# Optimization experiments

Hardware: AMD Instinct MI355X
Metric: run time of the kernel (lower is better)

## Reference

```python
import jax, jax.numpy as jnp
import numpy as np

N_EMBD = 1024
N_HEAD = 16
BLOCK_SIZE = 2048
NEG_INF = -1e10


def _rope_cache(head_dim, max_positions):
    # theta_i = 10000^{-2i/dim}, freqs[t, i] = t * theta_i
    theta = 1.0 / (10000.0 ** (jnp.arange(0, head_dim, 2, dtype=jnp.float32) / head_dim))
    freqs = jnp.arange(max_positions, dtype=jnp.float32)[:, None] * theta[None, :]
    return jnp.cos(freqs), jnp.sin(freqs)  # each (max_positions, head_dim//2)


def _apply_rope(x, cos, sin):
    # x: (B, nh, T, hs) interpreted as interleaved complex pairs
    B, nh, T, hs = x.shape
    xr = x.reshape(B, nh, T, hs // 2, 2)
    x0, x1 = xr[..., 0], xr[..., 1]
    c = cos[:T][None, None, :, :]
    s = sin[:T][None, None, :, :]
    o0 = x0 * c - x1 * s
    o1 = x0 * s + x1 * c
    return jnp.stack([o0, o1], axis=-1).reshape(B, nh, T, hs)


def setup_inputs() -> dict:
    key = jax.random.key(0)
    ks = jax.random.split(key, 9)
    B, T, C = 2, 2048, N_EMBD
    sc = 1.0 / np.sqrt(C)
    return {
        "x": jax.random.normal(ks[0], (B, T, C), jnp.float32),
        "Wq": jax.random.normal(ks[1], (C, C), jnp.float32) * sc,
        "bq": jax.random.normal(ks[2], (C,), jnp.float32) * 0.02,
        "Wk": jax.random.normal(ks[3], (C, C), jnp.float32) * sc,
        "bk": jax.random.normal(ks[4], (C,), jnp.float32) * 0.02,
        "Wv": jax.random.normal(ks[5], (C, C), jnp.float32) * sc,
        "bv": jax.random.normal(ks[6], (C,), jnp.float32) * 0.02,
        "Wp": jax.random.normal(ks[7], (C, C), jnp.float32) * sc,
        "bp": jax.random.normal(ks[8], (C,), jnp.float32) * 0.02,
    }


def reference(x, Wq, bq, Wk, bk, Wv, bv, Wp, bp):
    B, T, C = x.shape
    nh, hs = N_HEAD, C // N_HEAD

    def heads(W, b):
        return (x @ W.T + b).reshape(B, T, nh, hs).transpose(0, 2, 1, 3)

    q = heads(Wq, bq)
    k = heads(Wk, bk)
    v = heads(Wv, bv)

    cos, sin = _rope_cache(hs, BLOCK_SIZE)
    q = _apply_rope(q, cos, sin)
    k = _apply_rope(k, cos, sin)

    att = jnp.einsum("bhqd,bhkd->bhqk", q, k) * (1.0 / np.sqrt(hs))
    causal = jnp.tril(jnp.ones((T, T), dtype=bool))
    att = jnp.where(causal[None, None], att, NEG_INF)
    att = jax.nn.softmax(att, axis=-1)
    y = jnp.einsum("bhqk,bhkd->bhqd", att, v)
    y = y.transpose(0, 2, 1, 3).reshape(B, T, C)
    return y @ Wp.T + bp
```

## Files before the change

kernel.cpp:

```cpp
#include <hip/hip_runtime.h>

typedef __bf16 bf16;
typedef short  s16;
typedef s16   s16x8 __attribute__((ext_vector_type(8)));
typedef bf16  bf16x4 __attribute__((ext_vector_type(4)));
typedef float f32x4 __attribute__((ext_vector_type(4)));

#define B_SZ 2
#define T_SEQ 2048
#define C_DIM 1024
#define NH 16
#define HS 64
#define M_TOT (B_SZ * T_SEQ)

#define NEG_BIG (-30000.0f)
#define LOG2_10000 13.287712379549449f
#define Q_PRESCALE 0.18033688011112042f

__device__ __forceinline__ float san(float x) {
    unsigned u = __float_as_uint(x);
    return ((u & 0x7F800000u) == 0x7F800000u) ? 0.f : x;
}

__device__ __forceinline__ void load16_lds(const bf16* g, void* lds_base) {
    __builtin_amdgcn_global_load_lds(
        (const __attribute__((address_space(1))) void*)g,
        (__attribute__((address_space(3))) void*)lds_base, 16, 0, 0);
}

template <int N>
__device__ __forceinline__ float row_ror(float x) {
    return __int_as_float(__builtin_amdgcn_mov_dpp(
        __float_as_int(x), 0x120 + N, 0xf, 0xf, true));
}
__device__ __forceinline__ float rowsum16(float x) {
    x += row_ror<1>(x);
    x += row_ror<2>(x);
    x += row_ror<4>(x);
    x += row_ror<8>(x);
    return x;
}

__global__ __launch_bounds__(256) void cvt_bf16_kernel(
    const float* __restrict__ x,  const float* __restrict__ wq,
    const float* __restrict__ wk, const float* __restrict__ wv,
    const float* __restrict__ wp,
    bf16* __restrict__ xb, bf16* __restrict__ wqb, bf16* __restrict__ wkb,
    bf16* __restrict__ wvb, bf16* __restrict__ wpb)
{
    const int z = blockIdx.y;
    const float* src = (z == 0) ? x : (z == 1) ? wq : (z == 2) ? wk : (z == 3) ? wv : wp;
    bf16* dst = (z == 0) ? xb : (z == 1) ? wqb : (z == 2) ? wkb : (z == 3) ? wvb : wpb;
    const int n = (z == 0) ? (M_TOT * C_DIM) : (C_DIM * C_DIM);

    const int i = (blockIdx.x * 256 + threadIdx.x) * 4;
    if (i >= n) return;
    const float4 v = *(const float4*)(src + i);
    bf16x4 o;
    o[0] = (bf16)v.x; o[1] = (bf16)v.y; o[2] = (bf16)v.z; o[3] = (bf16)v.w;
    *(bf16x4*)(dst + i) = o;
}

__global__ __launch_bounds__(256) void rope_tab_kernel(float* __restrict__ cs,
                                                       float* __restrict__ sn)
{
    const int idx = blockIdx.x * 256 + threadIdx.x;
    const int t = idx >> 5, i = idx & 31;
    const float theta = __builtin_exp2f(-(float)(2 * i) * (LOG2_10000 / 64.f));
    const float a = (float)t * theta;
    cs[idx] = san(cosf(a));
    sn[idx] = san(sinf(a));
}

#define GEMM_CORE(Xp, Wp_)                                                     \
    const int t = threadIdx.x;                                                 \
    const int w = t >> 6;                                                      \
    const int lane = t & 63;                                                   \
    const int qd = lane >> 4;                                                  \
    const int r  = lane & 15;                                                  \
    const int wm = w & 1, wn = w >> 1;                                         \
    const int srow = t >> 2;                                                   \
    const int scol = (t & 3) * 8;                                              \
    const bf16* gA0 = (Xp) + (size_t)(m0 + srow) * C_DIM + scol;               \
    const bf16* gA1 = (Xp) + (size_t)(m0 + 64 + srow) * C_DIM + scol;          \
    const bf16* gB0 = (Wp_) + (size_t)(n0 + srow) * C_DIM + scol;              \
    const bf16* gB1 = (Wp_) + (size_t)(n0 + 64 + srow) * C_DIM + scol;         \
    char* ldsA0 = (char*)sA + (size_t)(w * 64) * 16;                           \
    char* ldsA1 = (char*)sA + (size_t)(256 + w * 64) * 16;                     \
    char* ldsB0 = (char*)sB + (size_t)(w * 64) * 16;                           \
    char* ldsB1 = (char*)sB + (size_t)(256 + w * 64) * 16;                     \
    f32x4 acc[4][4] = {};                                                      \
    for (int k0 = 0; k0 < C_DIM; k0 += 32) {                                   \
        __syncthreads();                                                       \
        load16_lds(gA0 + k0, ldsA0);                                           \
        load16_lds(gA1 + k0, ldsA1);                                           \
        load16_lds(gB0 + k0, ldsB0);                                           \
        load16_lds(gB1 + k0, ldsB1);                                           \
        __syncthreads();                                                       \
        s16x8 af[4], bfr[4];                                                   \
        _Pragma("unroll")                                                      \
        for (int mt = 0; mt < 4; mt++)                                         \
            af[mt] = *(const s16x8*)(sA + (wm * 64 + mt * 16 + r) * 32 + qd * 8); \
        _Pragma("unroll")                                                      \
        for (int nt = 0; nt < 4; nt++)                                         \
            bfr[nt] = *(const s16x8*)(sB + (wn * 64 + nt * 16 + r) * 32 + qd * 8); \
        _Pragma("unroll")                                                      \
        for (int mt = 0; mt < 4; mt++)                                         \
            _Pragma("unroll")                                                  \
            for (int nt = 0; nt < 4; nt++)                                     \
                acc[mt][nt] = __builtin_amdgcn_mfma_f32_16x16x32_bf16(         \
                    af[mt], bfr[nt], acc[mt][nt], 0, 0, 0);                    \
    }

__global__ __launch_bounds__(256) void qkv_gemm(
    const bf16* __restrict__ X,
    const bf16* __restrict__ Wq, const float* __restrict__ bq,
    const bf16* __restrict__ Wk, const float* __restrict__ bk,
    const bf16* __restrict__ Wv, const float* __restrict__ bv,
    const float* __restrict__ cs_tab, const float* __restrict__ sn_tab,
    bf16* __restrict__ q_ws, bf16* __restrict__ k_ws, bf16* __restrict__ vt_ws)
{
    __shared__ __attribute__((aligned(16))) bf16 sA[128 * 32];
    __shared__ __attribute__((aligned(16))) bf16 sB[128 * 32];

    const int mode = blockIdx.z;
    const bf16*  Wm   = (mode == 0) ? Wq : (mode == 1) ? Wk : Wv;
    const float* bias = (mode == 0) ? bq : (mode == 1) ? bk : bv;
    const int m0 = blockIdx.x * 128;
    const int n0 = blockIdx.y * 128;

    GEMM_CORE(X, Wm)

    if (mode == 2) {
        #pragma unroll
        for (int mt = 0; mt < 4; mt++) {
            const int mrow0 = m0 + wm * 64 + mt * 16 + qd * 4;
            const int bb = mrow0 >> 11;
            const int t0 = mrow0 & 2047;
            #pragma unroll
            for (int nt = 0; nt < 4; nt++) {
                const int col = n0 + wn * 64 + nt * 16 + r;
                const int h = col >> 6, d = col & 63;
                const float bv_ = bias[col];
                bf16x4 pk;
                #pragma unroll
                for (int reg = 0; reg < 4; reg++)
                    pk[reg] = (bf16)san(acc[mt][nt][reg] + bv_);
                *(bf16x4*)(vt_ws + ((size_t)(bb * NH + h) * HS + d) * T_SEQ + t0) = pk;
            }
        }
    } else {
        bf16* out = (mode == 0) ? q_ws : k_ws;
        const float post = (mode == 0) ? Q_PRESCALE : 1.0f;
        #pragma unroll
        for (int mt = 0; mt < 4; mt++) {
            const int mrow0 = m0 + wm * 64 + mt * 16 + qd * 4;
            const int bb = mrow0 >> 11;
            const int t0 = mrow0 & 2047;
            #pragma unroll
            for (int nt = 0; nt < 4; nt++) {
                const int col = n0 + wn * 64 + nt * 16 + r;
                const int h = col >> 6, d = col & 63;
                const int pi = d >> 1;
                const float bv_ = bias[col];
                #pragma unroll
                for (int reg = 0; reg < 4; reg++) {
                    const int tt = t0 + reg;
                    float v = san(acc[mt][nt][reg] + bv_);
                    float partner = __shfl_xor(v, 1);
                    float c = cs_tab[tt * 32 + pi];
                    float s = sn_tab[tt * 32 + pi];
                    float rot = (d & 1) ? (v * c + partner * s)
                                        : (v * c - partner * s);
                    out[((size_t)(bb * NH + h) * T_SEQ + tt) * HS + d] =
                        (bf16)san(rot * post);
                }
            }
        }
    }
}

__global__ __launch_bounds__(256) void proj_gemm(
    const bf16* __restrict__ Y, const bf16* __restrict__ Wp,
    const float* __restrict__ bp, float* __restrict__ out)
{
    __shared__ __attribute__((aligned(16))) bf16 sA[128 * 32];
    __shared__ __attribute__((aligned(16))) bf16 sB[128 * 32];

    const int m0 = blockIdx.x * 128;
    const int n0 = blockIdx.y * 128;

    GEMM_CORE(Y, Wp)

    #pragma unroll
    for (int mt = 0; mt < 4; mt++) {
        const int mrow0 = m0 + wm * 64 + mt * 16 + qd * 4;
        #pragma unroll
        for (int nt = 0; nt < 4; nt++) {
            const int col = n0 + wn * 64 + nt * 16 + r;
            const float bv_ = bp[col];
            #pragma unroll
            for (int reg = 0; reg < 4; reg++)
                out[(size_t)(mrow0 + reg) * C_DIM + col] = san(acc[mt][nt][reg] + bv_);
        }
    }
}

__global__ __launch_bounds__(256) void attn_kernel(
    const bf16* __restrict__ q_ws, const bf16* __restrict__ k_ws,
    const bf16* __restrict__ vt_ws, bf16* __restrict__ y_ws)
{
    __shared__ __attribute__((aligned(16))) bf16 sK[2][2][64][32];
    __shared__ __attribute__((aligned(16))) bf16 sV[2][2][64][32];
    __shared__ __attribute__((aligned(16))) bf16 sP[4][16][72];

    const int bx = blockIdx.x;
    const int bh = blockIdx.y;
    const int w    = threadIdx.x >> 6;
    const int lane = threadIdx.x & 63;
    const int qd = lane >> 4;
    const int r  = lane & 15;

    const bf16* Qb = q_ws + (size_t)bh * T_SEQ * HS;
    const bf16* Kb = k_ws + (size_t)bh * T_SEQ * HS;
    const bf16* Vb = vt_ws + (size_t)bh * HS * T_SEQ;

    const int srow = lane >> 2;
    const int scol = (lane & 3) * 8;
    const bf16* Kb_w = Kb + (size_t)(w * 16 + srow) * HS + scol;
    const bf16* Vb_w = Vb + (size_t)(w * 16 + srow) * T_SEQ + scol;

    bf16 (*pw)[72] = sP[w];
    const int bb = bh >> 4, h = bh & 15;

    #pragma unroll 1
    for (int phase = 0; phase < 2; phase++) {
        const int qt = phase ? bx : (T_SEQ / 64 - 1 - bx);
        const int q0 = qt * 64 + w * 16;

        s16x8 aq0 = *(const s16x8*)(Qb + (size_t)(q0 + r) * HS + qd * 8);
        s16x8 aq1 = *(const s16x8*)(Qb + (size_t)(q0 + r) * HS + 32 + qd * 8);

        f32x4 o[4] = {};
        float l_i[4];
        #pragma unroll
        for (int j = 0; j < 4; j++) l_i[j] = 0.f;

        __syncthreads();
        load16_lds(Kb_w,      &sK[0][0][w * 16][0]);
        load16_lds(Kb_w + 32, &sK[0][1][w * 16][0]);
        load16_lds(Vb_w,      &sV[0][0][w * 16][0]);
        load16_lds(Vb_w + 32, &sV[0][1][w * 16][0]);

        for (int kt = 0; kt <= qt; kt++) {
            const int cur = kt & 1;
            __syncthreads();

            if (kt < qt) {
                const bf16* kp = Kb_w + (size_t)(kt + 1) * 64 * HS;
                const bf16* vp = Vb_w + (kt + 1) * 64;
                load16_lds(kp,      &sK[cur ^ 1][0][w * 16][0]);
                load16_lds(kp + 32, &sK[cur ^ 1][1][w * 16][0]);
                load16_lds(vp,      &sV[cur ^ 1][0][w * 16][0]);
                load16_lds(vp + 32, &sV[cur ^ 1][1][w * 16][0]);
            }

            f32x4 s[4];
            #pragma unroll
            for (int nt = 0; nt < 4; nt++) {
                s16x8 b0 = *(const s16x8*)&sK[cur][0][nt * 16 + r][qd * 8];
                s16x8 b1 = *(const s16x8*)&sK[cur][1][nt * 16 + r][qd * 8];
                f32x4 z = {};
                z = __builtin_amdgcn_mfma_f32_16x16x32_bf16(aq0, b0, z, 0, 0, 0);
                z = __builtin_amdgcn_mfma_f32_16x16x32_bf16(aq1, b1, z, 0, 0, 0);
                s[nt] = z;
            }

            if (kt == qt) {
                #pragma unroll
                for (int nt = 0; nt < 4; nt++)
                    #pragma unroll
                    for (int reg = 0; reg < 4; reg++) {
                        const int qg = q0 + qd * 4 + reg;
                        const int kg = kt * 64 + nt * 16 + r;
                        s[nt][reg] = (kg <= qg) ? s[nt][reg] : NEG_BIG;
                    }
            }

            float rs[4];
            #pragma unroll
            for (int reg = 0; reg < 4; reg++) rs[reg] = 0.f;
            #pragma unroll
            for (int nt = 0; nt < 4; nt++)
                #pragma unroll
                for (int reg = 0; reg < 4; reg++) {
                    float p = __builtin_exp2f(s[nt][reg]);
                    s[nt][reg] = p;
                    rs[reg] += p;
                }
            #pragma unroll
            for (int reg = 0; reg < 4; reg++)
                l_i[reg] += rowsum16(rs[reg]);

            #pragma unroll
            for (int nt = 0; nt < 4; nt++)
                #pragma unroll
                for (int reg = 0; reg < 4; reg++)
                    pw[qd * 4 + reg][nt * 16 + r] = (bf16)s[nt][reg];

            s16x8 ap0 = *(const s16x8*)&pw[r][qd * 8];
            s16x8 ap1 = *(const s16x8*)&pw[r][32 + qd * 8];
            #pragma unroll
            for (int nt = 0; nt < 4; nt++) {
                s16x8 bv0 = *(const s16x8*)&sV[cur][0][nt * 16 + r][qd * 8];
                s16x8 bv1 = *(const s16x8*)&sV[cur][1][nt * 16 + r][qd * 8];
                o[nt] = __builtin_amdgcn_mfma_f32_16x16x32_bf16(ap0, bv0, o[nt], 0, 0, 0);
                o[nt] = __builtin_amdgcn_mfma_f32_16x16x32_bf16(ap1, bv1, o[nt], 0, 0, 0);
            }
        }

        #pragma unroll
        for (int reg = 0; reg < 4; reg++) {
            const int tq = q0 + qd * 4 + reg;
            const float inv = 1.f / fmaxf(l_i[reg], 1e-20f);
            bf16* dst = y_ws + ((size_t)(bb * T_SEQ + tq) * NH + h) * HS;
            #pragma unroll
            for (int nt = 0; nt < 4; nt++)
                dst[nt * 16 + r] = (bf16)san(o[nt][reg] * inv);
        }
    }
}

extern "C" void kernel_launch(void* const* d_in, const int* in_sizes, int n_in,
                              void* d_out, int out_size, void* d_ws, size_t ws_size,
                              hipStream_t stream)
{
    const size_t MB = 1024 * 1024;
    const size_t NEED = 40 * MB + 2 * 65536 * sizeof(float);
    if (ws_size < NEED || n_in < 9) return;

    const float* x  = (const float*)d_in[0];
    const float* Wq = (const float*)d_in[1];
    const float* bq = (const float*)d_in[2];
    const float* Wk = (const float*)d_in[3];
    const float* bk = (const float*)d_in[4];
    const float* Wv = (const float*)d_in[5];
    const float* bv = (const float*)d_in[6];
    const float* Wp = (const float*)d_in[7];
    const float* bp = (const float*)d_in[8];
    float* out = (float*)d_out;

    char* ws = (char*)d_ws;
    bf16*  q_ws   = (bf16*)(ws + 0 * MB);
    bf16*  k_ws   = (bf16*)(ws + 8 * MB);
    bf16*  vt_ws  = (bf16*)(ws + 16 * MB);
    bf16*  x_b    = (bf16*)(ws + 24 * MB);
    bf16*  y_ws   = (bf16*)(ws + 24 * MB);
    bf16*  Wq_b   = (bf16*)(ws + 32 * MB);
    bf16*  Wk_b   = (bf16*)(ws + 34 * MB);
    bf16*  Wv_b   = (bf16*)(ws + 36 * MB);
    bf16*  Wp_b   = (bf16*)(ws + 38 * MB);
    float* cs_tab = (float*)(ws + 40 * MB);
    float* sn_tab = cs_tab + 65536;

    cvt_bf16_kernel<<<dim3(M_TOT * C_DIM / 4 / 256, 5), 256, 0, stream>>>(
        x, Wq, Wk, Wv, Wp, x_b, Wq_b, Wk_b, Wv_b, Wp_b);
    rope_tab_kernel<<<dim3(65536 / 256), 256, 0, stream>>>(cs_tab, sn_tab);
    qkv_gemm<<<dim3(M_TOT / 128, C_DIM / 128, 3), 256, 0, stream>>>(
        x_b, Wq_b, bq, Wk_b, bk, Wv_b, bv, cs_tab, sn_tab, q_ws, k_ws, vt_ws);
    attn_kernel<<<dim3(T_SEQ / 128, B_SZ * NH), 256, 0, stream>>>(
        q_ws, k_ws, vt_ws, y_ws);
    proj_gemm<<<dim3(M_TOT / 128, C_DIM / 128), 256, 0, stream>>>(
        y_ws, Wp_b, bp, out);
}
```

Before: 216.9 us.

## Transpose attention MFMA operands so each lane owns one query row

Swaps the A/B operands of the QK^T and PV MFMAs, which transposes the output fragment so each lane holds one query row and four consecutive keys or dims. Per-tile row-sum DPP reductions are replaced by a per-lane accumulator that is reduced once with two shuffles at the end. P is written to LDS as packed bf16x4 stores instead of scalar stores, and output rows are stored as bf16x4 vectors. The cost being targeted is the per-iteration cross-lane reductions and scattered scalar LDS and global stores.

```diff
diff --git a/kernel.cpp b/kernel.cpp
--- a/kernel.cpp
+++ b/kernel.cpp
@@ -26,19 +26,6 @@
     __builtin_amdgcn_global_load_lds(
         (const __attribute__((address_space(1))) void*)g,
         (__attribute__((address_space(3))) void*)lds_base, 16, 0, 0);
-}
-
-template <int N>
-__device__ __forceinline__ float row_ror(float x) {
-    return __int_as_float(__builtin_amdgcn_mov_dpp(
-        __float_as_int(x), 0x120 + N, 0xf, 0xf, true));
-}
-__device__ __forceinline__ float rowsum16(float x) {
-    x += row_ror<1>(x);
-    x += row_ror<2>(x);
-    x += row_ror<4>(x);
-    x += row_ror<8>(x);
-    return x;
 }
 
 __global__ __launch_bounds__(256) void cvt_bf16_kernel(
@@ -242,9 +229,7 @@
         s16x8 aq1 = *(const s16x8*)(Qb + (size_t)(q0 + r) * HS + 32 + qd * 8);
 
         f32x4 o[4] = {};
-        float l_i[4];
-        #pragma unroll
-        for (int j = 0; j < 4; j++) l_i[j] = 0.f;
+        float l_lane = 0.f;
 
         __syncthreads();
         load16_lds(Kb_w,      &sK[0][0][w * 16][0]);
@@ -267,66 +252,63 @@
 
             f32x4 s[4];
             #pragma unroll
-            for (int nt = 0; nt < 4; nt++) {
-                s16x8 b0 = *(const s16x8*)&sK[cur][0][nt * 16 + r][qd * 8];
-                s16x8 b1 = *(const s16x8*)&sK[cur][1][nt * 16 + r][qd * 8];
+            for (int c = 0; c < 4; c++) {
+                s16x8 k0 = *(const s16x8*)&sK[cur][0][c * 16 + r][qd * 8];
+                s16x8 k1 = *(const s16x8*)&sK[cur][1][c * 16 + r][qd * 8];
                 f32x4 z = {};
-                z = __builtin_amdgcn_mfma_f32_16x16x32_bf16(aq0, b0, z, 0, 0, 0);
-                z = __builtin_amdgcn_mfma_f32_16x16x32_bf16(aq1, b1, z, 0, 0, 0);
-                s[nt] = z;
+                z = __builtin_amdgcn_mfma_f32_16x16x32_bf16(k0, aq0, z, 0, 0, 0);
+                z = __builtin_amdgcn_mfma_f32_16x16x32_bf16(k1, aq1, z, 0, 0, 0);
+                s[c] = z;
             }
 
             if (kt == qt) {
+                const int qg = q0 + r;
                 #pragma unroll
-                for (int nt = 0; nt < 4; nt++)
+                for (int c = 0; c < 4; c++)
                     #pragma unroll
                     for (int reg = 0; reg < 4; reg++) {
-                        const int qg = q0 + qd * 4 + reg;
-                        const int kg = kt * 64 + nt * 16 + r;
-                        s[nt][reg] = (kg <= qg) ? s[nt][reg] : NEG_BIG;
+                        const int kg = kt * 64 + c * 16 + qd * 4 + reg;
+                        s[c][reg] = (kg <= qg) ? s[c][reg] : NEG_BIG;
                     }
             }
 
-            float rs[4];
-            #pragma unroll
-            for (int reg = 0; reg < 4; reg++) rs[reg] = 0.f;
-            #pragma unroll
-            for (int nt = 0; nt < 4; nt++)
+            #pragma unroll
+            for (int c = 0; c < 4; c++) {
+                bf16x4 pk;
                 #pragma unroll
                 for (int reg = 0; reg < 4; reg++) {
-                    float p = __builtin_exp2f(s[nt][reg]);
-                    s[nt][reg] = p;
-                    rs[reg] += p;
+                    float p = __builtin_exp2f(s[c][reg]);
+                    l_lane += p;
+                    pk[reg] = (bf16)p;
                 }
-            #pragma unroll
-            for (int reg = 0; reg < 4; reg++)
-                l_i[reg] += rowsum16(rs[reg]);
-
-            #pragma unroll
-            for (int nt = 0; nt < 4; nt++)
-                #pragma unroll
-                for (int reg = 0; reg < 4; reg++)
-                    pw[qd * 4 + reg][nt * 16 + r] = (bf16)s[nt][reg];
+                *(bf16x4*)&pw[r][c * 16 + qd * 4] = pk;
+            }
 
             s16x8 ap0 = *(const s16x8*)&pw[r][qd * 8];
             s16x8 ap1 = *(const s16x8*)&pw[r][32 + qd * 8];
             #pragma unroll
             for (int nt = 0; nt < 4; nt++) {
-                s16x8 bv0 = *(const s16x8*)&sV[cur][0][nt * 16 + r][qd * 8];
-                s16x8 bv1 = *(const s16x8*)&sV[cur][1][nt * 16 + r][qd * 8];
-                o[nt] = __builtin_amdgcn_mfma_f32_16x16x32_bf16(ap0, bv0, o[nt], 0, 0, 0);
-                o[nt] = __builtin_amdgcn_mfma_f32_16x16x32_bf16(ap1, bv1, o[nt], 0, 0, 0);
-            }
-        }
-
+                s16x8 av0 = *(const s16x8*)&sV[cur][0][nt * 16 + r][qd * 8];
+                s16x8 av1 = *(const s16x8*)&sV[cur][1][nt * 16 + r][qd * 8];
+                o[nt] = __builtin_amdgcn_mfma_f32_16x16x32_bf16(av0, ap0, o[nt], 0, 0, 0);
+                o[nt] = __builtin_amdgcn_mfma_f32_16x16x32_bf16(av1, ap1, o[nt], 0, 0, 0);
+            }
+        }
+
+        float l = l_lane;
+        l += __shfl_xor(l, 16);
+        l += __shfl_xor(l, 32);
+        const float inv = 1.f / fmaxf(l, 1e-20f);
+
+        const int q = q0 + r;
+        bf16* dst = y_ws + ((size_t)(bb * T_SEQ + q) * NH + h) * HS;
         #pragma unroll
-        for (int reg = 0; reg < 4; reg++) {
-            const int tq = q0 + qd * 4 + reg;
-            const float inv = 1.f / fmaxf(l_i[reg], 1e-20f);
-            bf16* dst = y_ws + ((size_t)(bb * T_SEQ + tq) * NH + h) * HS;
-            #pragma unroll
-            for (int nt = 0; nt < 4; nt++)
-                dst[nt * 16 + r] = (bf16)san(o[nt][reg] * inv);
+        for (int nt = 0; nt < 4; nt++) {
+            bf16x4 pk;
+            #pragma unroll
+            for (int reg = 0; reg < 4; reg++)
+                pk[reg] = (bf16)san(o[nt][reg] * inv);
+            *(bf16x4*)(dst + nt * 16 + qd * 4) = pk;
         }
     }
 }
```

After: 212.1 us. 2.2% less time.
